# Kernel tuning notes

Hardware: AMD Instinct MI355X
Metric: run time of the kernel (lower is better)

Reference implementation:

```python
import jax, jax.numpy as jnp
import numpy as np

H = 8          # n_heads
D_HEAD = 64    # head_dim; scores scaled by sqrt(D_HEAD)


def setup_inputs() -> dict:
    key = jax.random.key(0)
    ks = jax.random.split(key, 9)
    B, S, Dm = 8, 1024, 512
    return {
        "input_Q": jax.random.normal(ks[0], (B, S, Dm), jnp.float32),
        "input_K": jax.random.normal(ks[1], (B, S, Dm), jnp.float32),
        "input_V": jax.random.normal(ks[2], (B, S, Dm), jnp.float32),
        "attn_mask": jax.random.randint(ks[3], (B, S, S), 0, 2).astype(bool),
        "edge_encoding": jax.random.normal(ks[4], (B, S, S), jnp.float32),
        "W_Q": jax.random.normal(ks[5], (Dm, Dm), jnp.float32) / np.sqrt(Dm),
        "W_K": jax.random.normal(ks[6], (Dm, Dm), jnp.float32) / np.sqrt(Dm),
        "W_V": jax.random.normal(ks[7], (Dm, Dm), jnp.float32) / np.sqrt(Dm),
        "W_fc": jax.random.normal(ks[8], (Dm, Dm), jnp.float32) / np.sqrt(Dm),
    }


def reference(input_Q, input_K, input_V, attn_mask, edge_encoding, W_Q, W_K, W_V, W_fc):
    B, S, Dm = input_Q.shape
    # project and split heads: [B, H, S, d_head]
    def heads(x, W):
        return (x @ W).reshape(B, S, H, D_HEAD).transpose(0, 2, 1, 3)
    Q = heads(input_Q, W_Q)
    K = heads(input_K, W_K)
    V = heads(input_V, W_V)
    scores = jnp.einsum("bhqd,bhkd->bhqk", Q, K) / np.sqrt(D_HEAD)
    scores = scores + edge_encoding[:, None, :, :]
    scores = jnp.where(attn_mask[:, None, :, :], jnp.float32(-1e9), scores)
    attn = jax.nn.softmax(scores, axis=-1)
    context = jnp.einsum("bhqk,bhkd->bhqd", attn, V)
    context = context.transpose(0, 2, 1, 3).reshape(B, S, Dm)
    output = context @ W_fc
    scores_avg = scores.sum(axis=1) / H  # [B, S, S]
    return output, scores_avg
```

## Files before the change

### kernel.cpp

```cpp
#include <hip/hip_runtime.h>
#include <math.h>

#define B_ 8
#define S_ 1024
#define DM 512
#define H_ 8
#define DH 64

typedef _Float16 h4 __attribute__((ext_vector_type(4)));
typedef _Float16 h8 __attribute__((ext_vector_type(8)));
typedef float f4 __attribute__((ext_vector_type(4)));

#define MFMA16(a, b, c) __builtin_amdgcn_mfma_f32_16x16x32_f16(a, b, c, 0, 0, 0)

__global__ __launch_bounds__(256) void cast_x(
    const float* __restrict__ x0, const float* __restrict__ x1,
    const float* __restrict__ x2, _Float16* __restrict__ y0,
    _Float16* __restrict__ y1, _Float16* __restrict__ y2) {
  const float* x = (blockIdx.y == 0) ? x0 : (blockIdx.y == 1) ? x1 : x2;
  _Float16* y = (blockIdx.y == 0) ? y0 : (blockIdx.y == 1) ? y1 : y2;
  size_t i = (size_t)blockIdx.x * 1024 + (size_t)threadIdx.x * 4;
  float4 v = *(const float4*)(x + i);
  h4 hv = {(_Float16)v.x, (_Float16)v.y, (_Float16)v.z, (_Float16)v.w};
  *(h4*)(y + i) = hv;
}

__global__ __launch_bounds__(256) void cast_w(
    const float* __restrict__ w0, const float* __restrict__ w1,
    const float* __restrict__ w2, const float* __restrict__ w3,
    _Float16* __restrict__ t0, _Float16* __restrict__ t1,
    _Float16* __restrict__ t2, _Float16* __restrict__ t3) {
  const float* W;
  _Float16* T;
  switch (blockIdx.z) {
    case 0: W = w0; T = t0; break;
    case 1: W = w1; T = t1; break;
    case 2: W = w2; T = t2; break;
    default: W = w3; T = t3; break;
  }
  __shared__ _Float16 ts[64][72];
  const int t = threadIdx.x;
  const int r = t >> 2, c0 = (t & 3) * 16;
  const int n0 = blockIdx.x * 64, k0 = blockIdx.y * 64;
#pragma unroll
  for (int i = 0; i < 4; i++) {
    float4 v = *(const float4*)&W[(size_t)(k0 + r) * 512 + n0 + c0 + i * 4];
    h4 hv = {(_Float16)v.x, (_Float16)v.y, (_Float16)v.z, (_Float16)v.w};
    *(h4*)&ts[r][c0 + i * 4] = hv;
  }
  __syncthreads();
  alignas(16) _Float16 outv[16];
#pragma unroll
  for (int i = 0; i < 16; i++) outv[i] = ts[c0 + i][r];
  *(uint4*)&T[(size_t)(n0 + r) * 512 + k0 + c0] = *(uint4*)&outv[0];
  *(uint4*)&T[(size_t)(n0 + r) * 512 + k0 + c0 + 8] = *(uint4*)&outv[8];
}

__global__ __launch_bounds__(256) void transpose_v(
    const _Float16* __restrict__ Vh, _Float16* __restrict__ Vth) {
  const int bh = blockIdx.y, b = bh >> 3, h = bh & 7;
  const int s0 = blockIdx.x * 64;
  __shared__ _Float16 ts[64][72];
  const int t = threadIdx.x;
  const int r = t >> 2, c0 = (t & 3) * 16;
  const size_t src = ((size_t)b * S_ + s0 + r) * DM + h * DH + c0;
  *(uint4*)&ts[r][c0] = *(const uint4*)&Vh[src];
  *(uint4*)&ts[r][c0 + 8] = *(const uint4*)&Vh[src + 8];
  __syncthreads();
  alignas(16) _Float16 outv[16];
#pragma unroll
  for (int i = 0; i < 16; i++) outv[i] = ts[c0 + i][r];
  const size_t dst = ((size_t)bh * 64 + r) * S_ + s0 + c0;
  *(uint4*)&Vth[dst] = *(uint4*)&outv[0];
  *(uint4*)&Vth[dst + 8] = *(uint4*)&outv[8];
}

template <bool F32OUT>
__global__ __launch_bounds__(256) void gemm_h(
    const _Float16* __restrict__ A, const _Float16* __restrict__ Bt,
    void* __restrict__ Cout, int M, int N, int K) {
  __shared__ _Float16 As[128][72], Bs[128][72];
  const int t = threadIdx.x, lane = t & 63, w = t >> 6;
  const int quad = lane >> 4, l16 = lane & 15;
  const int row0 = blockIdx.y * 128, col0 = blockIdx.x * 128;
  const int wm = (w & 1) * 64, wn = (w >> 1) * 64;
  const int gr = t >> 3, gc = (t & 7) * 8;
  f4 acc[4][4] = {};
  uint4 pa[4], pb[4];
#pragma unroll
  for (int i = 0; i < 4; i++) {
    pa[i] = *(const uint4*)&A[(size_t)(row0 + gr + 32 * i) * K + gc];
    pb[i] = *(const uint4*)&Bt[(size_t)(col0 + gr + 32 * i) * K + gc];
  }
  for (int k0 = 0; k0 < K; k0 += 64) {
    __syncthreads();
#pragma unroll
    for (int i = 0; i < 4; i++) {
      *(uint4*)&As[gr + 32 * i][gc] = pa[i];
      *(uint4*)&Bs[gr + 32 * i][gc] = pb[i];
    }
    __syncthreads();
    if (k0 + 64 < K) {
#pragma unroll
      for (int i = 0; i < 4; i++) {
        pa[i] = *(const uint4*)&A[(size_t)(row0 + gr + 32 * i) * K + k0 + 64 + gc];
        pb[i] = *(const uint4*)&Bt[(size_t)(col0 + gr + 32 * i) * K + k0 + 64 + gc];
      }
    }
    h8 af[4][2], bf[4][2];
#pragma unroll
    for (int m = 0; m < 4; m++) {
      af[m][0] = *(h8*)&As[wm + m * 16 + l16][quad * 8];
      af[m][1] = *(h8*)&As[wm + m * 16 + l16][32 + quad * 8];
    }
#pragma unroll
    for (int n = 0; n < 4; n++) {
      bf[n][0] = *(h8*)&Bs[wn + n * 16 + l16][quad * 8];
      bf[n][1] = *(h8*)&Bs[wn + n * 16 + l16][32 + quad * 8];
    }
#pragma unroll
    for (int m = 0; m < 4; m++)
#pragma unroll
      for (int n = 0; n < 4; n++) {
        acc[m][n] = MFMA16(af[m][0], bf[n][0], acc[m][n]);
        acc[m][n] = MFMA16(af[m][1], bf[n][1], acc[m][n]);
      }
  }
#pragma unroll
  for (int m = 0; m < 4; m++)
#pragma unroll
    for (int n = 0; n < 4; n++)
#pragma unroll
      for (int reg = 0; reg < 4; reg++) {
        size_t row = row0 + wm + m * 16 + quad * 4 + reg;
        size_t col = col0 + wn + n * 16 + l16;
        if (F32OUT)
          ((float*)Cout)[row * N + col] = acc[m][n][reg];
        else
          ((_Float16*)Cout)[row * N + col] = (_Float16)acc[m][n][reg];
      }
}

__global__ __launch_bounds__(256) void scores_mfma(
    const _Float16* __restrict__ Qh, const _Float16* __restrict__ Kh,
    const int* __restrict__ mask, const float* __restrict__ edge,
    float* __restrict__ out1, _Float16* __restrict__ Eh) {
  const int b = blockIdx.z;
  const int i0 = blockIdx.y * 128, j0 = blockIdx.x * 128;
  const _Float16* A = Qh + (size_t)b * S_ * DM;
  const _Float16* Bt = Kh + (size_t)b * S_ * DM;
  __shared__ _Float16 As[128][72], Bs[128][72];
  const int t = threadIdx.x, lane = t & 63, w = t >> 6;
  const int quad = lane >> 4, l16 = lane & 15;
  const int wm = (w & 1) * 64, wn = (w >> 1) * 64;
  const int gr = t >> 3, gc = (t & 7) * 8;
  f4 acc[4][4] = {};
  uint4 pa[4], pb[4];
#pragma unroll
  for (int i = 0; i < 4; i++) {
    pa[i] = *(const uint4*)&A[(size_t)(i0 + gr + 32 * i) * DM + gc];
    pb[i] = *(const uint4*)&Bt[(size_t)(j0 + gr + 32 * i) * DM + gc];
  }
  for (int k0 = 0; k0 < DM; k0 += 64) {
    __syncthreads();
#pragma unroll
    for (int i = 0; i < 4; i++) {
      *(uint4*)&As[gr + 32 * i][gc] = pa[i];
      *(uint4*)&Bs[gr + 32 * i][gc] = pb[i];
    }
    __syncthreads();
    if (k0 + 64 < DM) {
#pragma unroll
      for (int i = 0; i < 4; i++) {
        pa[i] = *(const uint4*)&A[(size_t)(i0 + gr + 32 * i) * DM + k0 + 64 + gc];
        pb[i] = *(const uint4*)&Bt[(size_t)(j0 + gr + 32 * i) * DM + k0 + 64 + gc];
      }
    }
    h8 af[4][2], bf[4][2];
#pragma unroll
    for (int m = 0; m < 4; m++) {
      af[m][0] = *(h8*)&As[wm + m * 16 + l16][quad * 8];
      af[m][1] = *(h8*)&As[wm + m * 16 + l16][32 + quad * 8];
    }
#pragma unroll
    for (int n = 0; n < 4; n++) {
      bf[n][0] = *(h8*)&Bs[wn + n * 16 + l16][quad * 8];
      bf[n][1] = *(h8*)&Bs[wn + n * 16 + l16][32 + quad * 8];
    }
#pragma unroll
    for (int m = 0; m < 4; m++)
#pragma unroll
      for (int n = 0; n < 4; n++) {
        acc[m][n] = MFMA16(af[m][0], bf[n][0], acc[m][n]);
        acc[m][n] = MFMA16(af[m][1], bf[n][1], acc[m][n]);
      }
  }
#pragma unroll
  for (int m = 0; m < 4; m++)
#pragma unroll
    for (int reg = 0; reg < 4; reg++) {
      size_t gi = i0 + wm + m * 16 + quad * 4 + reg;
      size_t rowb = ((size_t)b * S_ + gi) * S_;
#pragma unroll
      for (int n = 0; n < 4; n++) {
        size_t idx = rowb + j0 + wn + n * 16 + l16;
        int mk = mask[idx];
        float e = edge[idx];
        out1[idx] = mk ? -1e9f : (acc[m][n][reg] * (1.0f / 64.0f) + e);
        Eh[idx] = mk ? (_Float16)(-65504.0f) : (_Float16)e;
      }
    }
}

__global__ __launch_bounds__(256) void flash_mfma(
    const _Float16* __restrict__ Qh, const _Float16* __restrict__ Kh,
    const _Float16* __restrict__ Vth, const _Float16* __restrict__ Eh,
    _Float16* __restrict__ ctxh) {
  __shared__ _Float16 Ps[64][72], Ks[64][72], Vt[64][72];
  const int t = threadIdx.x, lane = t & 63, w = t >> 6;
  const int quad = lane >> 4, l16 = lane & 15;
  const int bh = blockIdx.y, b = bh >> 3, h = bh & 7;
  const int q0 = blockIdx.x * 64;
  const size_t bS = (size_t)b * S_;
  const int rqb = w * 16 + quad * 4;
  const int sr = t >> 3, sc = (t & 7) * 8;

  *(uint4*)&Ps[sr][sc] = *(const uint4*)&Qh[(bS + q0 + sr) * DM + h * DH + sc];
  *(uint4*)&Ps[sr + 32][sc] =
      *(const uint4*)&Qh[(bS + q0 + sr + 32) * DM + h * DH + sc];
  __syncthreads();
  h8 aq0 = *(h8*)&Ps[w * 16 + l16][quad * 8];
  h8 aq1 = *(h8*)&Ps[w * 16 + l16][32 + quad * 8];

  uint4 kv[4];
  kv[0] = *(const uint4*)&Kh[(bS + sr) * DM + h * DH + sc];
  kv[1] = *(const uint4*)&Kh[(bS + sr + 32) * DM + h * DH + sc];
  kv[2] = *(const uint4*)&Vth[((size_t)bh * 64 + sr) * S_ + sc];
  kv[3] = *(const uint4*)&Vth[((size_t)bh * 64 + sr + 32) * S_ + sc];
  _Float16 evh[16];
#pragma unroll
  for (int n = 0; n < 4; n++)
#pragma unroll
    for (int reg = 0; reg < 4; reg++)
      evh[n * 4 + reg] = Eh[(bS + q0 + rqb + reg) * S_ + n * 16 + l16];

  f4 acco[4] = {};
  float m_run[4], l_run[4];
#pragma unroll
  for (int r = 0; r < 4; r++) {
    m_run[r] = -INFINITY;
    l_run[r] = 0.f;
  }

  for (int kb = 0; kb < S_; kb += 64) {
    __syncthreads();
    *(uint4*)&Ks[sr][sc] = kv[0];
    *(uint4*)&Ks[sr + 32][sc] = kv[1];
    *(uint4*)&Vt[sr][sc] = kv[2];
    *(uint4*)&Vt[sr + 32][sc] = kv[3];
    __syncthreads();
    const int kn = kb + 64;
    _Float16 evn[16];
    if (kn < S_) {
      kv[0] = *(const uint4*)&Kh[(bS + kn + sr) * DM + h * DH + sc];
      kv[1] = *(const uint4*)&Kh[(bS + kn + sr + 32) * DM + h * DH + sc];
      kv[2] = *(const uint4*)&Vth[((size_t)bh * 64 + sr) * S_ + kn + sc];
      kv[3] = *(const uint4*)&Vth[((size_t)bh * 64 + sr + 32) * S_ + kn + sc];
#pragma unroll
      for (int n = 0; n < 4; n++)
#pragma unroll
        for (int reg = 0; reg < 4; reg++)
          evn[n * 4 + reg] = Eh[(bS + q0 + rqb + reg) * S_ + kn + n * 16 + l16];
    }
    f4 accs[4] = {};
#pragma unroll
    for (int n = 0; n < 4; n++) {
      h8 b0 = *(h8*)&Ks[n * 16 + l16][quad * 8];
      h8 b1 = *(h8*)&Ks[n * 16 + l16][32 + quad * 8];
      accs[n] = MFMA16(aq0, b0, accs[n]);
      accs[n] = MFMA16(aq1, b1, accs[n]);
    }
    float sv[4][4];
#pragma unroll
    for (int n = 0; n < 4; n++)
#pragma unroll
      for (int reg = 0; reg < 4; reg++)
        sv[n][reg] = accs[n][reg] * 0.125f + (float)evh[n * 4 + reg];
#pragma unroll
    for (int reg = 0; reg < 4; reg++) {
      float mx = fmaxf(fmaxf(sv[0][reg], sv[1][reg]),
                       fmaxf(sv[2][reg], sv[3][reg]));
#pragma unroll
      for (int off = 1; off < 16; off <<= 1)
        mx = fmaxf(mx, __shfl_xor(mx, off, 16));
      float mnew = fmaxf(m_run[reg], mx);
      float alpha = __expf(m_run[reg] - mnew);
      m_run[reg] = mnew;
      float psum = 0.f;
#pragma unroll
      for (int n = 0; n < 4; n++) {
        float p = __expf(sv[n][reg] - mnew);
        sv[n][reg] = p;
        psum += p;
      }
#pragma unroll
      for (int off = 1; off < 16; off <<= 1) psum += __shfl_xor(psum, off, 16);
      l_run[reg] = l_run[reg] * alpha + psum;
#pragma unroll
      for (int n = 0; n < 4; n++) acco[n][reg] *= alpha;
    }
#pragma unroll
    for (int n = 0; n < 4; n++)
#pragma unroll
      for (int reg = 0; reg < 4; reg++)
        Ps[rqb + reg][n * 16 + l16] = (_Float16)sv[n][reg];
    h8 ap0 = *(h8*)&Ps[w * 16 + l16][quad * 8];
    h8 ap1 = *(h8*)&Ps[w * 16 + l16][32 + quad * 8];
#pragma unroll
    for (int n = 0; n < 4; n++) {
      h8 bv0 = *(h8*)&Vt[n * 16 + l16][quad * 8];
      h8 bv1 = *(h8*)&Vt[n * 16 + l16][32 + quad * 8];
      acco[n] = MFMA16(ap0, bv0, acco[n]);
      acco[n] = MFMA16(ap1, bv1, acco[n]);
    }
    if (kn < S_) {
#pragma unroll
      for (int i = 0; i < 16; i++) evh[i] = evn[i];
    }
  }
#pragma unroll
  for (int n = 0; n < 4; n++)
#pragma unroll
    for (int reg = 0; reg < 4; reg++) {
      float o = acco[n][reg] / l_run[reg];
      ctxh[(bS + q0 + rqb + reg) * DM + h * DH + n * 16 + l16] = (_Float16)o;
    }
}

extern "C" void kernel_launch(void* const* d_in, const int* in_sizes, int n_in,
                              void* d_out, int out_size, void* d_ws,
                              size_t ws_size, hipStream_t stream) {
  const float* Xq = (const float*)d_in[0];
  const float* Xk = (const float*)d_in[1];
  const float* Xv = (const float*)d_in[2];
  const int* mask = (const int*)d_in[3];
  const float* edge = (const float*)d_in[4];
  const float* Wq = (const float*)d_in[5];
  const float* Wk = (const float*)d_in[6];
  const float* Wv = (const float*)d_in[7];
  const float* Wfc = (const float*)d_in[8];

  float* out0 = (float*)d_out;
  float* out1 = out0 + (size_t)B_ * S_ * DM;

  const size_t NE = (size_t)B_ * S_ * DM;
  char* ws = (char*)d_ws;
  _Float16* Qh = (_Float16*)ws;
  _Float16* Kh = Qh + NE;
  _Float16* Vh = Kh + NE;
  _Float16* Xhq = Vh + NE;
  _Float16* Xhk = Xhq + NE;
  _Float16* Xhv = Xhk + NE;
  _Float16* Wt = Xhv + NE;
  _Float16 *Wtq = Wt, *Wtk = Wt + 512 * 512, *Wtv = Wt + 2 * 512 * 512,
           *Wtf = Wt + 3 * 512 * 512;
  _Float16* Eh = Wt + 4 * 512 * 512;
  _Float16* ctxh = Xhq;
  _Float16* Vth = Xhk;

  dim3 blk(256);
  cast_x<<<dim3(4096, 3), blk, 0, stream>>>(Xq, Xk, Xv, Xhq, Xhk, Xhv);
  cast_w<<<dim3(8, 8, 4), blk, 0, stream>>>(Wq, Wk, Wv, Wfc, Wtq, Wtk, Wtv,
                                            Wtf);
  dim3 gp(DM / 128, (B_ * S_) / 128);
  gemm_h<false><<<gp, blk, 0, stream>>>(Xhq, Wtq, Qh, B_ * S_, DM, DM);
  gemm_h<false><<<gp, blk, 0, stream>>>(Xhk, Wtk, Kh, B_ * S_, DM, DM);
  scores_mfma<<<dim3(8, 8, 8), blk, 0, stream>>>(Qh, Kh, mask, edge, out1, Eh);
  gemm_h<false><<<gp, blk, 0, stream>>>(Xhv, Wtv, Vh, B_ * S_, DM, DM);
  transpose_v<<<dim3(16, 64), blk, 0, stream>>>(Vh, Vth);
  flash_mfma<<<dim3(16, 64), blk, 0, stream>>>(Qh, Kh, Vth, Eh, ctxh);
  gemm_h<true><<<gp, blk, 0, stream>>>(ctxh, Wtf, out0, B_ * S_, DM, DM);
}
```

Baseline: 425.8 us.

## Fuse QKV projections with V transpose, enlarge flash query tile, retile fc GEMM

Merges the three projection GEMMs into one launch whose V path writes directly in the transposed per-head layout, removing the separate transpose kernel and its round trip through memory. The flash attention kernel now handles 128 queries per block with two M-subtiles per wave, reusing each K/V tile for twice as many queries. The output projection uses 64-row tiles to launch more blocks. The trade-offs are more registers in flash, fewer flash blocks, and strided stores for the V layout.

```diff
diff --git a/kernel.cpp b/kernel.cpp
--- a/kernel.cpp
+++ b/kernel.cpp
@@ -56,29 +56,14 @@
   *(uint4*)&T[(size_t)(n0 + r) * 512 + k0 + c0 + 8] = *(uint4*)&outv[8];
 }
 
-__global__ __launch_bounds__(256) void transpose_v(
-    const _Float16* __restrict__ Vh, _Float16* __restrict__ Vth) {
-  const int bh = blockIdx.y, b = bh >> 3, h = bh & 7;
-  const int s0 = blockIdx.x * 64;
-  __shared__ _Float16 ts[64][72];
-  const int t = threadIdx.x;
-  const int r = t >> 2, c0 = (t & 3) * 16;
-  const size_t src = ((size_t)b * S_ + s0 + r) * DM + h * DH + c0;
-  *(uint4*)&ts[r][c0] = *(const uint4*)&Vh[src];
-  *(uint4*)&ts[r][c0 + 8] = *(const uint4*)&Vh[src + 8];
-  __syncthreads();
-  alignas(16) _Float16 outv[16];
-#pragma unroll
-  for (int i = 0; i < 16; i++) outv[i] = ts[c0 + i][r];
-  const size_t dst = ((size_t)bh * 64 + r) * S_ + s0 + c0;
-  *(uint4*)&Vth[dst] = *(uint4*)&outv[0];
-  *(uint4*)&Vth[dst + 8] = *(uint4*)&outv[8];
-}
-
-template <bool F32OUT>
-__global__ __launch_bounds__(256) void gemm_h(
-    const _Float16* __restrict__ A, const _Float16* __restrict__ Bt,
-    void* __restrict__ Cout, int M, int N, int K) {
+__global__ __launch_bounds__(256) void gemm_qkv(
+    const _Float16* __restrict__ Xq, const _Float16* __restrict__ Xk,
+    const _Float16* __restrict__ Xv, const _Float16* __restrict__ Wt,
+    _Float16* __restrict__ Qh, _Float16* __restrict__ Kh,
+    _Float16* __restrict__ Vth) {
+  const int z = blockIdx.z;
+  const _Float16* A = (z == 0) ? Xq : (z == 1) ? Xk : Xv;
+  const _Float16* Bt = Wt + (size_t)z * 512 * 512;
   __shared__ _Float16 As[128][72], Bs[128][72];
   const int t = threadIdx.x, lane = t & 63, w = t >> 6;
   const int quad = lane >> 4, l16 = lane & 15;
@@ -89,10 +74,10 @@
   uint4 pa[4], pb[4];
 #pragma unroll
   for (int i = 0; i < 4; i++) {
-    pa[i] = *(const uint4*)&A[(size_t)(row0 + gr + 32 * i) * K + gc];
-    pb[i] = *(const uint4*)&Bt[(size_t)(col0 + gr + 32 * i) * K + gc];
-  }
-  for (int k0 = 0; k0 < K; k0 += 64) {
+    pa[i] = *(const uint4*)&A[(size_t)(row0 + gr + 32 * i) * DM + gc];
+    pb[i] = *(const uint4*)&Bt[(size_t)(col0 + gr + 32 * i) * DM + gc];
+  }
+  for (int k0 = 0; k0 < DM; k0 += 64) {
     __syncthreads();
 #pragma unroll
     for (int i = 0; i < 4; i++) {
@@ -100,11 +85,11 @@
       *(uint4*)&Bs[gr + 32 * i][gc] = pb[i];
     }
     __syncthreads();
-    if (k0 + 64 < K) {
+    if (k0 + 64 < DM) {
 #pragma unroll
       for (int i = 0; i < 4; i++) {
-        pa[i] = *(const uint4*)&A[(size_t)(row0 + gr + 32 * i) * K + k0 + 64 + gc];
-        pb[i] = *(const uint4*)&Bt[(size_t)(col0 + gr + 32 * i) * K + k0 + 64 + gc];
+        pa[i] = *(const uint4*)&A[(size_t)(row0 + gr + 32 * i) * DM + k0 + 64 + gc];
+        pb[i] = *(const uint4*)&Bt[(size_t)(col0 + gr + 32 * i) * DM + k0 + 64 + gc];
       }
     }
     h8 af[4][2], bf[4][2];
@@ -126,18 +111,94 @@
         acc[m][n] = MFMA16(af[m][1], bf[n][1], acc[m][n]);
       }
   }
-#pragma unroll
-  for (int m = 0; m < 4; m++)
+  if (z < 2) {
+    _Float16* C = (z == 0) ? Qh : Kh;
+#pragma unroll
+    for (int m = 0; m < 4; m++)
+#pragma unroll
+      for (int n = 0; n < 4; n++)
+#pragma unroll
+        for (int reg = 0; reg < 4; reg++) {
+          size_t row = row0 + wm + m * 16 + quad * 4 + reg;
+          size_t col = col0 + wn + n * 16 + l16;
+          C[row * DM + col] = (_Float16)acc[m][n][reg];
+        }
+  } else {
+#pragma unroll
+    for (int m = 0; m < 4; m++)
+#pragma unroll
+      for (int n = 0; n < 4; n++) {
+        int row = row0 + wm + m * 16 + quad * 4;
+        int b = row >> 10, s = row & 1023;
+        int col = col0 + wn + n * 16 + l16;
+        int h = col >> 6, d = col & 63;
+        h4 vv = {(_Float16)acc[m][n][0], (_Float16)acc[m][n][1],
+                 (_Float16)acc[m][n][2], (_Float16)acc[m][n][3]};
+        *(h4*)&Vth[((size_t)(b * 8 + h) * 64 + d) * S_ + s] = vv;
+      }
+  }
+}
+
+__global__ __launch_bounds__(256) void gemm_fc(
+    const _Float16* __restrict__ A, const _Float16* __restrict__ Bt,
+    float* __restrict__ C) {
+  __shared__ _Float16 As[64][72], Bs[128][72];
+  const int t = threadIdx.x, lane = t & 63, w = t >> 6;
+  const int quad = lane >> 4, l16 = lane & 15;
+  const int row0 = blockIdx.y * 64, col0 = blockIdx.x * 128;
+  const int wm = (w & 1) * 32, wn = (w >> 1) * 64;
+  const int gr = t >> 3, gc = (t & 7) * 8;
+  f4 acc[2][4] = {};
+  uint4 pa[2], pb[4];
+#pragma unroll
+  for (int i = 0; i < 2; i++)
+    pa[i] = *(const uint4*)&A[(size_t)(row0 + gr + 32 * i) * DM + gc];
+#pragma unroll
+  for (int i = 0; i < 4; i++)
+    pb[i] = *(const uint4*)&Bt[(size_t)(col0 + gr + 32 * i) * DM + gc];
+  for (int k0 = 0; k0 < DM; k0 += 64) {
+    __syncthreads();
+#pragma unroll
+    for (int i = 0; i < 2; i++) *(uint4*)&As[gr + 32 * i][gc] = pa[i];
+#pragma unroll
+    for (int i = 0; i < 4; i++) *(uint4*)&Bs[gr + 32 * i][gc] = pb[i];
+    __syncthreads();
+    if (k0 + 64 < DM) {
+#pragma unroll
+      for (int i = 0; i < 2; i++)
+        pa[i] = *(const uint4*)&A[(size_t)(row0 + gr + 32 * i) * DM + k0 + 64 + gc];
+#pragma unroll
+      for (int i = 0; i < 4; i++)
+        pb[i] = *(const uint4*)&Bt[(size_t)(col0 + gr + 32 * i) * DM + k0 + 64 + gc];
+    }
+    h8 af[2][2], bf[4][2];
+#pragma unroll
+    for (int m = 0; m < 2; m++) {
+      af[m][0] = *(h8*)&As[wm + m * 16 + l16][quad * 8];
+      af[m][1] = *(h8*)&As[wm + m * 16 + l16][32 + quad * 8];
+    }
+#pragma unroll
+    for (int n = 0; n < 4; n++) {
+      bf[n][0] = *(h8*)&Bs[wn + n * 16 + l16][quad * 8];
+      bf[n][1] = *(h8*)&Bs[wn + n * 16 + l16][32 + quad * 8];
+    }
+#pragma unroll
+    for (int m = 0; m < 2; m++)
+#pragma unroll
+      for (int n = 0; n < 4; n++) {
+        acc[m][n] = MFMA16(af[m][0], bf[n][0], acc[m][n]);
+        acc[m][n] = MFMA16(af[m][1], bf[n][1], acc[m][n]);
+      }
+  }
+#pragma unroll
+  for (int m = 0; m < 2; m++)
 #pragma unroll
     for (int n = 0; n < 4; n++)
 #pragma unroll
       for (int reg = 0; reg < 4; reg++) {
         size_t row = row0 + wm + m * 16 + quad * 4 + reg;
         size_t col = col0 + wn + n * 16 + l16;
-        if (F32OUT)
-          ((float*)Cout)[row * N + col] = acc[m][n][reg];
-        else
-          ((_Float16*)Cout)[row * N + col] = (_Float16)acc[m][n][reg];
+        C[row * DM + col] = acc[m][n][reg];
       }
 }
 
@@ -216,41 +277,51 @@
     const _Float16* __restrict__ Qh, const _Float16* __restrict__ Kh,
     const _Float16* __restrict__ Vth, const _Float16* __restrict__ Eh,
     _Float16* __restrict__ ctxh) {
-  __shared__ _Float16 Ps[64][72], Ks[64][72], Vt[64][72];
+  __shared__ _Float16 Ps[128][72], Ks[64][72], Vt[64][72];
   const int t = threadIdx.x, lane = t & 63, w = t >> 6;
   const int quad = lane >> 4, l16 = lane & 15;
   const int bh = blockIdx.y, b = bh >> 3, h = bh & 7;
-  const int q0 = blockIdx.x * 64;
+  const int q0 = blockIdx.x * 128;
   const size_t bS = (size_t)b * S_;
-  const int rqb = w * 16 + quad * 4;
   const int sr = t >> 3, sc = (t & 7) * 8;
-
-  *(uint4*)&Ps[sr][sc] = *(const uint4*)&Qh[(bS + q0 + sr) * DM + h * DH + sc];
-  *(uint4*)&Ps[sr + 32][sc] =
-      *(const uint4*)&Qh[(bS + q0 + sr + 32) * DM + h * DH + sc];
+  const int qw = w * 32;
+
+#pragma unroll
+  for (int i = 0; i < 4; i++)
+    *(uint4*)&Ps[sr + 32 * i][sc] =
+        *(const uint4*)&Qh[(bS + q0 + sr + 32 * i) * DM + h * DH + sc];
   __syncthreads();
-  h8 aq0 = *(h8*)&Ps[w * 16 + l16][quad * 8];
-  h8 aq1 = *(h8*)&Ps[w * 16 + l16][32 + quad * 8];
+  h8 aq[2][2];
+#pragma unroll
+  for (int m = 0; m < 2; m++)
+#pragma unroll
+    for (int k = 0; k < 2; k++)
+      aq[m][k] = *(h8*)&Ps[qw + m * 16 + l16][k * 32 + quad * 8];
 
   uint4 kv[4];
   kv[0] = *(const uint4*)&Kh[(bS + sr) * DM + h * DH + sc];
   kv[1] = *(const uint4*)&Kh[(bS + sr + 32) * DM + h * DH + sc];
   kv[2] = *(const uint4*)&Vth[((size_t)bh * 64 + sr) * S_ + sc];
   kv[3] = *(const uint4*)&Vth[((size_t)bh * 64 + sr + 32) * S_ + sc];
-  _Float16 evh[16];
-#pragma unroll
-  for (int n = 0; n < 4; n++)
-#pragma unroll
-    for (int reg = 0; reg < 4; reg++)
-      evh[n * 4 + reg] = Eh[(bS + q0 + rqb + reg) * S_ + n * 16 + l16];
-
-  f4 acco[4] = {};
-  float m_run[4], l_run[4];
-#pragma unroll
-  for (int r = 0; r < 4; r++) {
-    m_run[r] = -INFINITY;
-    l_run[r] = 0.f;
-  }
+  _Float16 evh[32];
+#pragma unroll
+  for (int m = 0; m < 2; m++)
+#pragma unroll
+    for (int n = 0; n < 4; n++)
+#pragma unroll
+      for (int reg = 0; reg < 4; reg++)
+        evh[m * 16 + n * 4 + reg] =
+            Eh[(bS + q0 + qw + m * 16 + quad * 4 + reg) * S_ + n * 16 + l16];
+
+  f4 acco[2][4] = {};
+  float m_run[2][4], l_run[2][4];
+#pragma unroll
+  for (int m = 0; m < 2; m++)
+#pragma unroll
+    for (int r = 0; r < 4; r++) {
+      m_run[m][r] = -INFINITY;
+      l_run[m][r] = 0.f;
+    }
 
   for (int kb = 0; kb < S_; kb += 64) {
     __syncthreads();
@@ -260,81 +331,107 @@
     *(uint4*)&Vt[sr + 32][sc] = kv[3];
     __syncthreads();
     const int kn = kb + 64;
-    _Float16 evn[16];
+    _Float16 evn[32];
     if (kn < S_) {
       kv[0] = *(const uint4*)&Kh[(bS + kn + sr) * DM + h * DH + sc];
       kv[1] = *(const uint4*)&Kh[(bS + kn + sr + 32) * DM + h * DH + sc];
       kv[2] = *(const uint4*)&Vth[((size_t)bh * 64 + sr) * S_ + kn + sc];
       kv[3] = *(const uint4*)&Vth[((size_t)bh * 64 + sr + 32) * S_ + kn + sc];
 #pragma unroll
-      for (int n = 0; n < 4; n++)
-#pragma unroll
-        for (int reg = 0; reg < 4; reg++)
-          evn[n * 4 + reg] = Eh[(bS + q0 + rqb + reg) * S_ + kn + n * 16 + l16];
-    }
-    f4 accs[4] = {};
+      for (int m = 0; m < 2; m++)
+#pragma unroll
+        for (int n = 0; n < 4; n++)
+#pragma unroll
+          for (int reg = 0; reg < 4; reg++)
+            evn[m * 16 + n * 4 + reg] =
+                Eh[(bS + q0 + qw + m * 16 + quad * 4 + reg) * S_ + kn +
+                   n * 16 + l16];
+    }
+    f4 accs[2][4] = {};
 #pragma unroll
     for (int n = 0; n < 4; n++) {
       h8 b0 = *(h8*)&Ks[n * 16 + l16][quad * 8];
       h8 b1 = *(h8*)&Ks[n * 16 + l16][32 + quad * 8];
-      accs[n] = MFMA16(aq0, b0, accs[n]);
-      accs[n] = MFMA16(aq1, b1, accs[n]);
-    }
-    float sv[4][4];
-#pragma unroll
-    for (int n = 0; n < 4; n++)
-#pragma unroll
-      for (int reg = 0; reg < 4; reg++)
-        sv[n][reg] = accs[n][reg] * 0.125f + (float)evh[n * 4 + reg];
-#pragma unroll
-    for (int reg = 0; reg < 4; reg++) {
-      float mx = fmaxf(fmaxf(sv[0][reg], sv[1][reg]),
-                       fmaxf(sv[2][reg], sv[3][reg]));
-#pragma unroll
-      for (int off = 1; off < 16; off <<= 1)
-        mx = fmaxf(mx, __shfl_xor(mx, off, 16));
-      float mnew = fmaxf(m_run[reg], mx);
-      float alpha = __expf(m_run[reg] - mnew);
-      m_run[reg] = mnew;
-      float psum = 0.f;
-#pragma unroll
-      for (int n = 0; n < 4; n++) {
-        float p = __expf(sv[n][reg] - mnew);
-        sv[n][reg] = p;
-        psum += p;
-      }
-#pragma unroll
-      for (int off = 1; off < 16; off <<= 1) psum += __shfl_xor(psum, off, 16);
-      l_run[reg] = l_run[reg] * alpha + psum;
-#pragma unroll
-      for (int n = 0; n < 4; n++) acco[n][reg] *= alpha;
-    }
-#pragma unroll
-    for (int n = 0; n < 4; n++)
-#pragma unroll
-      for (int reg = 0; reg < 4; reg++)
-        Ps[rqb + reg][n * 16 + l16] = (_Float16)sv[n][reg];
-    h8 ap0 = *(h8*)&Ps[w * 16 + l16][quad * 8];
-    h8 ap1 = *(h8*)&Ps[w * 16 + l16][32 + quad * 8];
-#pragma unroll
-    for (int n = 0; n < 4; n++) {
-      h8 bv0 = *(h8*)&Vt[n * 16 + l16][quad * 8];
-      h8 bv1 = *(h8*)&Vt[n * 16 + l16][32 + quad * 8];
-      acco[n] = MFMA16(ap0, bv0, acco[n]);
-      acco[n] = MFMA16(ap1, bv1, acco[n]);
+#pragma unroll
+      for (int m = 0; m < 2; m++) {
+        accs[m][n] = MFMA16(aq[m][0], b0, accs[m][n]);
+        accs[m][n] = MFMA16(aq[m][1], b1, accs[m][n]);
+      }
+    }
+    float sv[2][4][4];
+#pragma unroll
+    for (int m = 0; m < 2; m++)
+#pragma unroll
+      for (int n = 0; n < 4; n++)
+#pragma unroll
+        for (int reg = 0; reg < 4; reg++)
+          sv[m][n][reg] =
+              accs[m][n][reg] * 0.125f + (float)evh[m * 16 + n * 4 + reg];
+#pragma unroll
+    for (int m = 0; m < 2; m++)
+#pragma unroll
+      for (int reg = 0; reg < 4; reg++) {
+        float mx = fmaxf(fmaxf(sv[m][0][reg], sv[m][1][reg]),
+                         fmaxf(sv[m][2][reg], sv[m][3][reg]));
+#pragma unroll
+        for (int off = 1; off < 16; off <<= 1)
+          mx = fmaxf(mx, __shfl_xor(mx, off, 16));
+        float mnew = fmaxf(m_run[m][reg], mx);
+        float alpha = __expf(m_run[m][reg] - mnew);
+        m_run[m][reg] = mnew;
+        float psum = 0.f;
+#pragma unroll
+        for (int n = 0; n < 4; n++) {
+          float p = __expf(sv[m][n][reg] - mnew);
+          sv[m][n][reg] = p;
+          psum += p;
+        }
+#pragma unroll
+        for (int off = 1; off < 16; off <<= 1)
+          psum += __shfl_xor(psum, off, 16);
+        l_run[m][reg] = l_run[m][reg] * alpha + psum;
+#pragma unroll
+        for (int d = 0; d < 4; d++) acco[m][d][reg] *= alpha;
+      }
+#pragma unroll
+    for (int m = 0; m < 2; m++)
+#pragma unroll
+      for (int n = 0; n < 4; n++)
+#pragma unroll
+        for (int reg = 0; reg < 4; reg++)
+          Ps[qw + m * 16 + quad * 4 + reg][n * 16 + l16] =
+              (_Float16)sv[m][n][reg];
+    h8 ap[2][2];
+#pragma unroll
+    for (int m = 0; m < 2; m++)
+#pragma unroll
+      for (int k = 0; k < 2; k++)
+        ap[m][k] = *(h8*)&Ps[qw + m * 16 + l16][k * 32 + quad * 8];
+#pragma unroll
+    for (int d = 0; d < 4; d++) {
+      h8 bv0 = *(h8*)&Vt[d * 16 + l16][quad * 8];
+      h8 bv1 = *(h8*)&Vt[d * 16 + l16][32 + quad * 8];
+#pragma unroll
+      for (int m = 0; m < 2; m++) {
+        acco[m][d] = MFMA16(ap[m][0], bv0, acco[m][d]);
+        acco[m][d] = MFMA16(ap[m][1], bv1, acco[m][d]);
+      }
     }
     if (kn < S_) {
 #pragma unroll
-      for (int i = 0; i < 16; i++) evh[i] = evn[i];
-    }
-  }
-#pragma unroll
-  for (int n = 0; n < 4; n++)
-#pragma unroll
-    for (int reg = 0; reg < 4; reg++) {
-      float o = acco[n][reg] / l_run[reg];
-      ctxh[(bS + q0 + rqb + reg) * DM + h * DH + n * 16 + l16] = (_Float16)o;
-    }
+      for (int i = 0; i < 32; i++) evh[i] = evn[i];
+    }
+  }
+#pragma unroll
+  for (int m = 0; m < 2; m++)
+#pragma unroll
+    for (int d = 0; d < 4; d++)
+#pragma unroll
+      for (int reg = 0; reg < 4; reg++) {
+        float o = acco[m][d][reg] / l_run[m][reg];
+        ctxh[(bS + q0 + qw + m * 16 + quad * 4 + reg) * DM + h * DH + d * 16 +
+             l16] = (_Float16)o;
+      }
 }
 
 extern "C" void kernel_launch(void* const* d_in, const int* in_sizes, int n_in,
@@ -357,27 +454,22 @@
   char* ws = (char*)d_ws;
   _Float16* Qh = (_Float16*)ws;
   _Float16* Kh = Qh + NE;
-  _Float16* Vh = Kh + NE;
-  _Float16* Xhq = Vh + NE;
+  _Float16* Vth = Kh + NE;
+  _Float16* Xhq = Vth + NE;
   _Float16* Xhk = Xhq + NE;
   _Float16* Xhv = Xhk + NE;
   _Float16* Wt = Xhv + NE;
-  _Float16 *Wtq = Wt, *Wtk = Wt + 512 * 512, *Wtv = Wt + 2 * 512 * 512,
-           *Wtf = Wt + 3 * 512 * 512;
+  _Float16* Wtf = Wt + 3 * 512 * 512;
   _Float16* Eh = Wt + 4 * 512 * 512;
   _Float16* ctxh = Xhq;
-  _Float16* Vth = Xhk;
 
   dim3 blk(256);
   cast_x<<<dim3(4096, 3), blk, 0, stream>>>(Xq, Xk, Xv, Xhq, Xhk, Xhv);
-  cast_w<<<dim3(8, 8, 4), blk, 0, stream>>>(Wq, Wk, Wv, Wfc, Wtq, Wtk, Wtv,
+  cast_w<<<dim3(8, 8, 4), blk, 0, stream>>>(Wq, Wk, Wv, Wfc, Wt,
+                                            Wt + 512 * 512, Wt + 2 * 512 * 512,
                                             Wtf);
-  dim3 gp(DM / 128, (B_ * S_) / 128);
-  gemm_h<false><<<gp, blk, 0, stream>>>(Xhq, Wtq, Qh, B_ * S_, DM, DM);
-  gemm_h<false><<<gp, blk, 0, stream>>>(Xhk, Wtk, Kh, B_ * S_, DM, DM);
+  gemm_qkv<<<dim3(4, 64, 3), blk, 0, stream>>>(Xhq, Xhk, Xhv, Wt, Qh, Kh, Vth);
   scores_mfma<<<dim3(8, 8, 8), blk, 0, stream>>>(Qh, Kh, mask, edge, out1, Eh);
-  gemm_h<false><<<gp, blk, 0, stream>>>(Xhv, Wtv, Vh, B_ * S_, DM, DM);
-  transpose_v<<<dim3(16, 64), blk, 0, stream>>>(Vh, Vth);
-  flash_mfma<<<dim3(16, 64), blk, 0, stream>>>(Qh, Kh, Vth, Eh, ctxh);
-  gemm_h<true><<<gp, blk, 0, stream>>>(ctxh, Wtf, out0, B_ * S_, DM, DM);
-}
+  flash_mfma<<<dim3(8, 64), blk, 0, stream>>>(Qh, Kh, Vth, Eh, ctxh);
+  gemm_fc<<<dim3(4, 128), blk, 0, stream>>>(ctxh, Wtf, out0);
+}
```

Result: faster. 402.6 us (-5.5%).
